# Kernel optimization log

Hardware: AMD Instinct MI355X
Metric: run time of the kernel (lower is better)

## Reference

```python
import jax, jax.numpy as jnp
import numpy as np
from jax import lax

T = 10.0
DT = 0.1
N_STEPS = 100          # T / dt
NUM_VALS = 10          # number of time-indexed Linear layers
STEPS_PER_SLAB = N_STEPS // NUM_VALS  # 10


def setup_inputs() -> dict:
    key = jax.random.key(0)
    k1, k2, k3 = jax.random.split(key, 3)
    B, D = 1024, 1024
    x = jax.random.normal(k1, (B, D), dtype=jnp.float32)
    # per-time-slab Linear weights/biases (nn.Linear-like scale)
    W = jax.random.normal(k2, (NUM_VALS, D, D), dtype=jnp.float32) * (1.0 / np.sqrt(D))
    b = jax.random.normal(k3, (NUM_VALS, D), dtype=jnp.float32) * 0.01
    return {"x": x, "W": W, "b": b}


def reference(x, W, b):
    # Euler integration of x' = tanh(W_k x + b_k), k = floor(t / (T/num_vals)).
    # Step n has t = n*dt, so k = n // STEPS_PER_SLAB (static schedule).
    ks = jnp.arange(N_STEPS, dtype=jnp.int32) // STEPS_PER_SLAB  # [100]

    def step(h, k):
        # Linear: h @ W_k^T + b_k, then tanh (architecture='inside')
        f = jnp.tanh(h @ W[k].T + b[k])
        h = h + DT * f
        return h, h

    features, traj_tail = lax.scan(step, x, ks)
    # trajectory at linspace(0, T, 101) == Euler grid: prepend initial state
    traj = jnp.concatenate([x[None], traj_tail], axis=0)  # [101, B, D]
    # final_layer=False: forward returns (pred, traj) with pred = features
    return features, traj
```

## Files before the change

### kernel.cpp

```cpp
#include <hip/hip_runtime.h>

#define D 1024
#define DT 0.1f

typedef __attribute__((ext_vector_type(8))) __bf16 bf16x8;
typedef __attribute__((ext_vector_type(4))) float floatx4;

__device__ __forceinline__ unsigned short f2bf(float f) {
  unsigned int u = __builtin_bit_cast(unsigned int, f);
  u = u + 0x7fffu + ((u >> 16) & 1u);
  return (unsigned short)(u >> 16);
}
__device__ __forceinline__ float bf2f(unsigned short b) {
  return __builtin_bit_cast(float, ((unsigned int)b) << 16);
}

__device__ __forceinline__ void gload_lds16(const void* g, void* l) {
  __builtin_amdgcn_global_load_lds(
      (const __attribute__((address_space(1))) void*)g,
      (__attribute__((address_space(3))) void*)l, 16, 0, 0);
}

__device__ __forceinline__ float fast_tanh(float x) {
  float ax = __builtin_fabsf(x);
  float e  = __expf(-2.0f * ax);
  float y  = (1.0f - e) * __builtin_amdgcn_rcpf(1.0f + e);
  return __builtin_copysignf(y, x);
}

__global__ void __launch_bounds__(256) split_kernel(
    const float* __restrict__ src, float* __restrict__ copy_dst,
    unsigned short* __restrict__ hi, unsigned short* __restrict__ lo) {
  const int i = blockIdx.x * blockDim.x + threadIdx.x;
  float4 v = ((const float4*)src)[i];
  if (copy_dst) ((float4*)copy_dst)[i] = v;
  ushort4 h, l;
  h.x = f2bf(v.x); l.x = f2bf(v.x - bf2f(h.x));
  h.y = f2bf(v.y); l.y = f2bf(v.y - bf2f(h.y));
  h.z = f2bf(v.z); l.z = f2bf(v.z - bf2f(h.z));
  h.w = f2bf(v.w); l.w = f2bf(v.w - bf2f(h.w));
  ((ushort4*)hi)[i] = h;
  ((ushort4*)lo)[i] = l;
}

__global__ void __launch_bounds__(512) step_kernel(
    const unsigned short* __restrict__ Ah, const unsigned short* __restrict__ Al,
    const unsigned short* __restrict__ Bh, const unsigned short* __restrict__ Bl,
    const float* __restrict__ bias,
    const float* __restrict__ hprev, float* __restrict__ hnext,
    unsigned short* __restrict__ Nh, unsigned short* __restrict__ Nl,
    float* __restrict__ feat) {
  __shared__ unsigned short lds[4 * 4 * 64 * 64];
  char* ldsb = (char*)lds;

  const int tid  = threadIdx.x;
  const int lane = tid & 63;
  const int wave = tid >> 6;
  const int wr   = wave >> 1;
  const int wc   = wave & 1;

  const int xcd = blockIdx.x & 7;
  const int j8  = blockIdx.x >> 3;
  const int rt  = ((xcd >> 1) << 2) | (j8 >> 3);
  const int ct  = ((xcd & 1) << 3) | (j8 & 7);
  const int row0 = rt << 6;
  const int col0 = ct << 6;

  const int quad = lane >> 4;
  const int l15  = lane & 15;

  const int srow = lane >> 3;
  const int sgrp = (lane & 7) ^ srow;
  const long aoff = (long)(row0 + wave * 8 + srow) * D + sgrp * 8;
  const long boff = (long)(col0 + wave * 8 + srow) * D + sgrp * 8;
  const unsigned short* gAh = Ah + aoff;
  const unsigned short* gAl = Al + aoff;
  const unsigned short* gBh = Bh + boff;
  const unsigned short* gBl = Bl + boff;
  const int sw = wave * 1024;

  const int ecol = col0 + (wc << 5) + l15;
  const int erow = row0 + (wr << 4) + (quad << 2);
  float hp0[4], hp1[4];
#pragma unroll
  for (int r = 0; r < 4; ++r) {
    const long i0 = (long)(erow + r) * D + ecol;
    hp0[r] = hprev[i0];
    hp1[r] = hprev[i0 + 16];
  }
  const float b0 = bias[ecol];
  const float b1 = bias[ecol + 16];

  const int Ra  = (wr << 4) | l15;
  const int Rb0 = (wc << 5) | l15;
  const int Rb1 = Rb0 + 16;
  const int x7  = lane & 7;

  floatx4 acc0 = {0.f, 0.f, 0.f, 0.f};
  floatx4 acc1 = {0.f, 0.f, 0.f, 0.f};

  auto stage = [&](int ck, int bo) {
    const int kk = ck << 6;
    gload_lds16(gAh + kk, ldsb + bo + 0     + sw);
    gload_lds16(gAl + kk, ldsb + bo + 8192  + sw);
    gload_lds16(gBh + kk, ldsb + bo + 16384 + sw);
    gload_lds16(gBl + kk, ldsb + bo + 24576 + sw);
  };

  stage(0, 0 << 15);
  stage(1, 1 << 15);
  stage(2, 2 << 15);

  for (int c = 0; c < 16; ++c) {
    if (c <= 13)      asm volatile("s_waitcnt vmcnt(8)" ::: "memory");
    else if (c == 14) asm volatile("s_waitcnt vmcnt(4)" ::: "memory");
    else              asm volatile("s_waitcnt vmcnt(0)" ::: "memory");
    asm volatile("s_barrier" ::: "memory");
    if (c < 13) stage(c + 3, ((c + 3) & 3) << 15);
    const char* base = ldsb + ((c & 3) << 15);
#pragma unroll
    for (int kc = 0; kc < 2; ++kc) {
      const int gs = (((kc << 2) | quad) ^ x7) << 4;
      bf16x8 ah  = *(const bf16x8*)(base + 0     + Ra  * 128 + gs);
      bf16x8 al  = *(const bf16x8*)(base + 8192  + Ra  * 128 + gs);
      bf16x8 bh0 = *(const bf16x8*)(base + 16384 + Rb0 * 128 + gs);
      bf16x8 bl0 = *(const bf16x8*)(base + 24576 + Rb0 * 128 + gs);
      bf16x8 bh1 = *(const bf16x8*)(base + 16384 + Rb1 * 128 + gs);
      bf16x8 bl1 = *(const bf16x8*)(base + 24576 + Rb1 * 128 + gs);
      acc0 = __builtin_amdgcn_mfma_f32_16x16x32_bf16(ah, bh0, acc0, 0, 0, 0);
      acc1 = __builtin_amdgcn_mfma_f32_16x16x32_bf16(ah, bh1, acc1, 0, 0, 0);
      acc0 = __builtin_amdgcn_mfma_f32_16x16x32_bf16(al, bh0, acc0, 0, 0, 0);
      acc1 = __builtin_amdgcn_mfma_f32_16x16x32_bf16(al, bh1, acc1, 0, 0, 0);
      acc0 = __builtin_amdgcn_mfma_f32_16x16x32_bf16(ah, bl0, acc0, 0, 0, 0);
      acc1 = __builtin_amdgcn_mfma_f32_16x16x32_bf16(ah, bl1, acc1, 0, 0, 0);
    }
  }

  const bool wf = (feat != nullptr);
#pragma unroll
  for (int r = 0; r < 4; ++r) {
    const long i0 = (long)(erow + r) * D + ecol;
    {
      float f  = fast_tanh(acc0[r] + b0);
      float hn = hp0[r] + DT * f;
      hnext[i0] = hn;
      unsigned short hb = f2bf(hn);
      Nh[i0] = hb;
      Nl[i0] = f2bf(hn - bf2f(hb));
      if (wf) feat[i0] = hn;
    }
    {
      const long i1 = i0 + 16;
      float f  = fast_tanh(acc1[r] + b1);
      float hn = hp1[r] + DT * f;
      hnext[i1] = hn;
      unsigned short hb = f2bf(hn);
      Nh[i1] = hb;
      Nl[i1] = f2bf(hn - bf2f(hb));
      if (wf) feat[i1] = hn;
    }
  }
}

extern "C" void kernel_launch(void* const* d_in, const int* in_sizes, int n_in,
                              void* d_out, int out_size, void* d_ws, size_t ws_size,
                              hipStream_t stream) {
  const float* x = (const float*)d_in[0];
  const float* W = (const float*)d_in[1];
  const float* b = (const float*)d_in[2];
  float* out  = (float*)d_out;
  float* feat = out;
  float* traj = out + (size_t)D * D;

  const size_t M = (size_t)D * D;
  unsigned short* ws = (unsigned short*)d_ws;
  const int splitBlocks = (int)(M / 4 / 256);

  const bool big = ws_size >= (size_t)48 * 1024 * 1024;

  if (big) {
    unsigned short* wh_all = ws;
    unsigned short* wl_all = wh_all + 10 * M;
    unsigned short* hbuf   = wl_all + 10 * M;
    unsigned short* hh[2] = {hbuf, hbuf + 2 * M};
    unsigned short* hl[2] = {hbuf + M, hbuf + 3 * M};

    split_kernel<<<splitBlocks * 10, 256, 0, stream>>>(W, (float*)nullptr, wh_all, wl_all);
    split_kernel<<<splitBlocks, 256, 0, stream>>>(x, traj, hh[0], hl[0]);

    for (int n = 0; n < 100; ++n) {
      const int k = n / 10;
      step_kernel<<<256, 512, 0, stream>>>(
          hh[n & 1], hl[n & 1], wh_all + (size_t)k * M, wl_all + (size_t)k * M,
          b + (size_t)k * D,
          traj + (size_t)n * M, traj + (size_t)(n + 1) * M,
          hh[(n + 1) & 1], hl[(n + 1) & 1],
          (n == 99) ? feat : nullptr);
    }
  } else {
    unsigned short* wh    = ws;
    unsigned short* wl    = wh + M;
    unsigned short* hbuf  = wl + M;
    unsigned short* hh[2] = {hbuf, hbuf + 2 * M};
    unsigned short* hl[2] = {hbuf + M, hbuf + 3 * M};

    split_kernel<<<splitBlocks, 256, 0, stream>>>(x, traj, hh[0], hl[0]);
    for (int k = 0; k < 10; ++k) {
      split_kernel<<<splitBlocks, 256, 0, stream>>>(W + k * M, (float*)nullptr, wh, wl);
      for (int s = 0; s < 10; ++s) {
        const int n = k * 10 + s;
        step_kernel<<<256, 512, 0, stream>>>(
            hh[n & 1], hl[n & 1], wh, wl, b + (size_t)k * D,
            traj + (size_t)n * M, traj + (size_t)(n + 1) * M,
            hh[(n + 1) & 1], hl[(n + 1) & 1],
            (n == 99) ? feat : nullptr);
      }
    }
  }
}
```

Before: 1.508 ms.

## Load A operand directly into registers instead of staging through LDS

The h (A) tiles are now fetched straight from global memory into registers, using a three-deep register prefetch ring. Only the W (B) tiles still go through LDS via global_load_lds, which halves the LDS footprint per stage and removes the A-side LDS reads. The main loop is fully unrolled and the vmcnt wait counts are retuned for the new mix of outstanding loads. The cost is more VGPR pressure, and since each 16-row A slice is loaded once per wave, the two column waves both fetch it, which doubles A global traffic.

```diff
diff --git a/kernel.cpp b/kernel.cpp
--- a/kernel.cpp
+++ b/kernel.cpp
@@ -50,7 +50,7 @@
     const float* __restrict__ hprev, float* __restrict__ hnext,
     unsigned short* __restrict__ Nh, unsigned short* __restrict__ Nl,
     float* __restrict__ feat) {
-  __shared__ unsigned short lds[4 * 4 * 64 * 64];
+  __shared__ unsigned short lds[4 * 8192];
   char* ldsb = (char*)lds;
 
   const int tid  = threadIdx.x;
@@ -68,16 +68,18 @@
 
   const int quad = lane >> 4;
   const int l15  = lane & 15;
+  const int x7   = lane & 7;
 
   const int srow = lane >> 3;
-  const int sgrp = (lane & 7) ^ srow;
-  const long aoff = (long)(row0 + wave * 8 + srow) * D + sgrp * 8;
+  const int sgrp = x7 ^ srow;
   const long boff = (long)(col0 + wave * 8 + srow) * D + sgrp * 8;
-  const unsigned short* gAh = Ah + aoff;
-  const unsigned short* gAl = Al + aoff;
   const unsigned short* gBh = Bh + boff;
   const unsigned short* gBl = Bl + boff;
   const int sw = wave * 1024;
+
+  const int Ra = (wr << 4) | l15;
+  const unsigned short* gA_h = Ah + (long)(row0 + Ra) * D + (quad << 3);
+  const unsigned short* gA_l = Al + (long)(row0 + Ra) * D + (quad << 3);
 
   const int ecol = col0 + (wc << 5) + l15;
   const int erow = row0 + (wr << 4) + (quad << 2);
@@ -91,42 +93,53 @@
   const float b0 = bias[ecol];
   const float b1 = bias[ecol + 16];
 
-  const int Ra  = (wr << 4) | l15;
   const int Rb0 = (wc << 5) | l15;
   const int Rb1 = Rb0 + 16;
-  const int x7  = lane & 7;
 
   floatx4 acc0 = {0.f, 0.f, 0.f, 0.f};
   floatx4 acc1 = {0.f, 0.f, 0.f, 0.f};
 
-  auto stage = [&](int ck, int bo) {
+  bf16x8 pa[3][4];
+
+  auto stageB = [&](int ck) {
     const int kk = ck << 6;
-    gload_lds16(gAh + kk, ldsb + bo + 0     + sw);
-    gload_lds16(gAl + kk, ldsb + bo + 8192  + sw);
-    gload_lds16(gBh + kk, ldsb + bo + 16384 + sw);
-    gload_lds16(gBl + kk, ldsb + bo + 24576 + sw);
+    const int bo = (ck & 3) << 14;
+    gload_lds16(gBh + kk, ldsb + bo + 0    + sw);
+    gload_lds16(gBl + kk, ldsb + bo + 8192 + sw);
   };
-
-  stage(0, 0 << 15);
-  stage(1, 1 << 15);
-  stage(2, 2 << 15);
-
+  auto loadA = [&](int ck) {
+    const int k0 = ck << 6;
+    bf16x8* d = pa[ck % 3];
+    d[0] = *(const bf16x8*)(gA_h + k0);
+    d[1] = *(const bf16x8*)(gA_h + k0 + 32);
+    d[2] = *(const bf16x8*)(gA_l + k0);
+    d[3] = *(const bf16x8*)(gA_l + k0 + 32);
+  };
+
+  stageB(0); stageB(1);
+  asm volatile("" ::: "memory");
+  loadA(0); loadA(1);
+  asm volatile("" ::: "memory");
+  stageB(2);
+
+#pragma unroll
   for (int c = 0; c < 16; ++c) {
-    if (c <= 13)      asm volatile("s_waitcnt vmcnt(8)" ::: "memory");
-    else if (c == 14) asm volatile("s_waitcnt vmcnt(4)" ::: "memory");
-    else              asm volatile("s_waitcnt vmcnt(0)" ::: "memory");
+    if (c < 15) asm volatile("s_waitcnt vmcnt(6)" ::: "memory");
+    else        asm volatile("s_waitcnt vmcnt(0)" ::: "memory");
     asm volatile("s_barrier" ::: "memory");
-    if (c < 13) stage(c + 3, ((c + 3) & 3) << 15);
-    const char* base = ldsb + ((c & 3) << 15);
+    if (c <= 13) loadA(c + 2);
+    if (c <= 12) stageB(c + 3);
+    const char* base = ldsb + ((c & 3) << 14);
+    const bf16x8* A = pa[c % 3];
 #pragma unroll
     for (int kc = 0; kc < 2; ++kc) {
       const int gs = (((kc << 2) | quad) ^ x7) << 4;
-      bf16x8 ah  = *(const bf16x8*)(base + 0     + Ra  * 128 + gs);
-      bf16x8 al  = *(const bf16x8*)(base + 8192  + Ra  * 128 + gs);
-      bf16x8 bh0 = *(const bf16x8*)(base + 16384 + Rb0 * 128 + gs);
-      bf16x8 bl0 = *(const bf16x8*)(base + 24576 + Rb0 * 128 + gs);
-      bf16x8 bh1 = *(const bf16x8*)(base + 16384 + Rb1 * 128 + gs);
-      bf16x8 bl1 = *(const bf16x8*)(base + 24576 + Rb1 * 128 + gs);
+      bf16x8 ah  = A[kc];
+      bf16x8 al  = A[2 + kc];
+      bf16x8 bh0 = *(const bf16x8*)(base + 0    + Rb0 * 128 + gs);
+      bf16x8 bl0 = *(const bf16x8*)(base + 8192 + Rb0 * 128 + gs);
+      bf16x8 bh1 = *(const bf16x8*)(base + 0    + Rb1 * 128 + gs);
+      bf16x8 bl1 = *(const bf16x8*)(base + 8192 + Rb1 * 128 + gs);
       acc0 = __builtin_amdgcn_mfma_f32_16x16x32_bf16(ah, bh0, acc0, 0, 0, 0);
       acc1 = __builtin_amdgcn_mfma_f32_16x16x32_bf16(ah, bh1, acc1, 0, 0, 0);
       acc0 = __builtin_amdgcn_mfma_f32_16x16x32_bf16(al, bh0, acc0, 0, 0, 0);
```

Result: slower. 2.516 ms (+66.9%).
